# Kernel optimization log

Measured on AMD Instinct MI355X. Metric: run time of the kernel, lower is better.

## Reference

```python
import jax, jax.numpy as jnp
import numpy as np

SEQ, D_IN, H, D_OUT = 8192, 256, 2048, 64


def setup_inputs() -> dict:
    key = jax.random.key(0)
    ks = jax.random.split(key, 9)
    s = 1.0 / np.sqrt(H)  # torch LSTM/Linear init scale
    u = lambda k, shape: jax.random.uniform(k, shape, jnp.float32, -s, s)
    return {
        "x": jax.random.normal(ks[0], (SEQ, D_IN), jnp.float32),
        "hprev": jax.random.normal(ks[1], (1, 1, H), jnp.float32),
        "cprev": jax.random.normal(ks[2], (1, 1, H), jnp.float32),
        "W_ih": u(ks[3], (4 * H, D_IN)),   # gate order: i, f, g, o
        "W_hh": u(ks[4], (4 * H, H)),
        "b_ih": u(ks[5], (4 * H,)),
        "b_hh": u(ks[6], (4 * H,)),
        "W_fc": u(ks[7], (D_OUT, H)),
        "b_fc": u(ks[8], (D_OUT,)),
    }


def _lstm_forward(x, h0, c0, W_ih, W_hh, b_ih, b_hh, W_fc, b_fc):
    # precompute input contributions for all timesteps: [T, 4H]
    xg = x @ W_ih.T + (b_ih + b_hh)
    W_hh_T = W_hh.T  # [H, 4H]

    def step(carry, xg_t):
        h, c = carry
        z = xg_t + h @ W_hh_T  # [4H]
        i, f, g, o = jnp.split(z, 4)
        i = jax.nn.sigmoid(i)
        f = jax.nn.sigmoid(f)
        g = jnp.tanh(g)
        o = jax.nn.sigmoid(o)
        c = f * c + i * g
        h = o * jnp.tanh(c)
        return (h, c), h

    (hT, cT), hs = jax.lax.scan(step, (h0, c0), xg)
    out = jax.nn.sigmoid(hs @ W_fc.T + b_fc)  # [T, D_OUT]
    return out, hT, cT


def reference(x, hprev, cprev, W_ih, W_hh, b_ih, b_hh, W_fc, b_fc):
    out, hT, cT = _lstm_forward(
        x, hprev[0, 0], cprev[0, 0], W_ih, W_hh, b_ih, b_hh, W_fc, b_fc
    )
    return out, hT[None, None, :], cT[None, None, :]
```

## Files before the change

### kernel.cpp

```cpp
#include <hip/hip_runtime.h>
#include <stdint.h>

typedef __fp16 f16x2 __attribute__((ext_vector_type(2)));
typedef __fp16 f16x8 __attribute__((ext_vector_type(8)));
typedef uint32_t u32x4 __attribute__((ext_vector_type(4)));
typedef unsigned long long ull;

#define SEQ  8192
#define HDIM 2048
#define DIN  256
#define DOUT 64

__device__ __forceinline__ f16x2 pk(float lo, float hi) {
    return __builtin_amdgcn_cvt_pkrtz(lo, hi);
}
__device__ __forceinline__ f16x2 pk2(float2 v) { return pk(v.x, v.y); }
__device__ __forceinline__ uint32_t h2u(f16x2 h) { return __builtin_bit_cast(uint32_t, h); }
__device__ __forceinline__ float sigf(float x) { return 1.0f / (1.0f + __expf(-x)); }
__device__ __forceinline__ float tanh_fast(float x) { return 2.0f * sigf(2.0f * x) - 1.0f; }

__device__ __forceinline__ int skH(int j) { return j + 4 * (j >> 7); }
__device__ __forceinline__ int skX(int j) { return j + 4 * (j >> 4); }

__device__ __forceinline__ void ld32_sc1(const ull* p, u32x4& a, u32x4& b) {
    asm volatile("global_load_dwordx4 %0, %2, off sc1\n\t"
                 "global_load_dwordx4 %1, %2, off offset:16 sc1\n\t"
                 "s_waitcnt vmcnt(0)"
                 : "=&v"(a), "=&v"(b) : "v"(p) : "memory");
}
__device__ __forceinline__ u32x4 ld_ctr4(const uint32_t* p) {
    u32x4 v;
    asm volatile("global_load_dwordx4 %0, %1, off sc1\n\t"
                 "s_waitcnt vmcnt(0)"
                 : "=&v"(v) : "v"(p) : "memory");
    return v;
}

__global__ void __launch_bounds__(256, 1)
lstm_persist(const float2* __restrict__ x2,
             const float2* __restrict__ hprev2,
             const float*  __restrict__ cprev,
             const float*  __restrict__ wih,
             const float*  __restrict__ whh,
             const float*  __restrict__ bih,
             const float*  __restrict__ bhh,
             const float2* __restrict__ wfc2,
             const float*  __restrict__ bfc,
             float* __restrict__ out,
             uint32_t* __restrict__ hs_w,
             ull* __restrict__ htag,
             uint32_t* __restrict__ ctr)
{
    const int tid = threadIdx.x;
    const int b   = blockIdx.x;
    const int wv  = tid >> 6;
    const int l   = tid & 63;
    const int g   = l >> 4;
    const int p   = (l >> 3) & 1;
    const int c   = l & 7;

    __shared__ __align__(16) uint32_t smem[12672];
    uint32_t* ldsH0 = smem;
    uint32_t* ldsH1 = smem + 1056;
    uint32_t* ldsX0 = smem + 2112;
    uint32_t* ldsX1 = smem + 2272;
    uint32_t* hsl = smem;
    uint32_t* wfl = smem + 4224;

    uint32_t* hs_priv = hs_w + (size_t)b * 32 * 1024;

    const int unit = 8 * b + 2 * wv + p;
    const int r    = g * 2048 + unit;
    f16x2 wh[128];
    {
        const float4* ptr = (const float4*)(whh + (size_t)r * 2048 + 256 * c);
#pragma unroll
        for (int q = 0; q < 64; ++q) {
            float4 v = ptr[q];
            wh[2*q+0] = pk(v.x, v.y);
            wh[2*q+1] = pk(v.z, v.w);
        }
    }
    f16x2 wx[16];
    {
        const float4* ptr = (const float4*)(wih + (size_t)r * 256 + 32 * c);
#pragma unroll
        for (int q = 0; q < 8; ++q) {
            float4 v = ptr[q];
            wx[2*q+0] = pk(v.x, v.y);
            wx[2*q+1] = pk(v.z, v.w);
        }
    }
#pragma unroll
    for (int k = 0; k < 4; ++k) {
        int j = tid + 256 * k;
        ldsH0[skH(j)] = h2u(pk2(hprev2[j]));
    }
    if (tid < 128) ldsX0[skX(tid)] = h2u(pk2(x2[tid]));
    float2 xw = {0.f, 0.f};
    if (tid < 128) xw = x2[128 + tid];

    float cloc = cprev[unit];
    float hloc = 0.f;
    const float bsum = bih[r] + bhh[r];
    u32x4 prev_pays = {0, 0, 0, 0};
    int  prev_row = 0;
    bool prev_own = false;
    const ull deadline = __builtin_amdgcn_s_memrealtime() + 60000000ull;
    __syncthreads();

    for (int t = 0; t < SEQ; ++t) {
        uint32_t* ldsH  = (t & 1) ? ldsH1 : ldsH0;
        uint32_t* ldsXc = (t & 1) ? ldsX1 : ldsX0;
        uint32_t* ldsXn = (t & 1) ? ldsX0 : ldsX1;

        float accs[8];
#pragma unroll
        for (int q = 0; q < 8; ++q) accs[q] = 0.f;
        {
            const f16x8* xp = (const f16x8*)(ldsXc + 20 * c);
#pragma unroll
            for (int q = 0; q < 4; ++q) {
                f16x8 xv = xp[q];
#pragma unroll
                for (int d = 0; d < 4; ++d) {
                    f16x2 hv = {xv[2*d], xv[2*d+1]};
                    int idx = 4 * q + d;
                    accs[idx & 7] = __builtin_amdgcn_fdot2(wx[idx], hv, accs[idx & 7], false);
                }
            }
        }
        if (tid < 128 && t + 1 < SEQ) ldsXn[skX(tid)] = h2u(pk2(xw));

        if (t > 0) {
            const int par = t & 1;
            const uint32_t target = (uint32_t)((t + (t & 1)) >> 1) * 8u;
            const uint32_t* cbase = ctr + (size_t)par * 8 * 128;
            int spins = 0;
            for (;;) {
                bool ok = true;
                if (l < 8) {
                    u32x4 v = ld_ctr4(cbase + (size_t)l * 128);
                    ok = (v[0] >= target) && (v[1] >= target) &&
                         (v[2] >= target) && (v[3] >= target);
                }
                if (__all(ok)) break;
                if (spins++ > 0) {
                    if (__builtin_amdgcn_s_memrealtime() > deadline) break;
                    __builtin_amdgcn_s_sleep(1);
                }
            }
            const ull* mb = htag + (size_t)par * 1024 + 4 * tid;
            u32x4 qa, qb;
            for (;;) {
                ld32_sc1(mb, qa, qb);
                if (qa[1] == (uint32_t)t && qa[3] == (uint32_t)t &&
                    qb[1] == (uint32_t)t && qb[3] == (uint32_t)t) break;
                if (__builtin_amdgcn_s_memrealtime() > deadline) break;
                __builtin_amdgcn_s_sleep(1);
            }
            u32x4 pays = {qa[0], qa[2], qb[0], qb[2]};
            *(u32x4*)(ldsH + skH(4 * tid)) = pays;
            if (prev_own)
                *(u32x4*)(hs_priv + (size_t)(prev_row & 31) * 1024 + 4 * tid) = prev_pays;
            prev_pays = pays;
            prev_row  = t - 1;
            prev_own  = ((t - 1) >> 5) == b;
        }
        if (tid < 128 && t + 2 < SEQ) xw = x2[(size_t)(t + 2) * 128 + tid];

        __syncthreads();

        {
            const f16x8* hp = (const f16x8*)(ldsH + 132 * c);
#pragma unroll
            for (int q = 0; q < 32; ++q) {
                f16x8 hv8 = hp[q];
#pragma unroll
                for (int d = 0; d < 4; ++d) {
                    f16x2 hh = {hv8[2*d], hv8[2*d+1]};
                    int idx = 4 * q + d;
                    accs[idx & 7] = __builtin_amdgcn_fdot2(wh[idx], hh, accs[idx & 7], false);
                }
            }
        }
        float acc = ((accs[0] + accs[1]) + (accs[2] + accs[3]))
                  + ((accs[4] + accs[5]) + (accs[6] + accs[7]));
        acc += __shfl_xor(acc, 1);
        acc += __shfl_xor(acc, 2);
        acc += __shfl_xor(acc, 4);

        float z = acc + bsum;
        const bool isg = (g == 2);
        float s  = sigf(isg ? 2.0f * z : z);
        float val = isg ? (2.0f * s - 1.0f) : s;
        const int p8 = l & 8;
        float iv = __shfl(val, p8 + 0);
        float fv = __shfl(val, p8 + 16);
        float gv = __shfl(val, p8 + 32);
        float ov = __shfl(val, p8 + 48);
        cloc = fv * cloc + iv * gv;
        hloc = ov * tanh_fast(cloc);

        float h0 = __shfl(hloc, 0);
        float h1 = __shfl(hloc, 8);
        uint32_t pay = h2u(pk(h0, h1));
        if (l == 0) {
            ull tv = ((ull)(uint32_t)(t + 1) << 32) | (ull)pay;
            __hip_atomic_store(htag + (size_t)((t + 1) & 1) * 1024 + 4 * b + wv,
                               tv, __ATOMIC_RELAXED, __HIP_MEMORY_SCOPE_AGENT);
            if (wv == 0)
                atomicAdd(ctr + ((size_t)((t + 1) & 1) * 8 + (b & 7)) * 128 + ((b >> 3) & 3), 1u);
        }
    }

    if (prev_own)
        *(u32x4*)(hs_priv + (size_t)(prev_row & 31) * 1024 + 4 * tid) = prev_pays;

    if (l == 0 || l == 8) {
        out[(size_t)SEQ * DOUT + unit]        = hloc;
        out[(size_t)SEQ * DOUT + HDIM + unit] = cloc;
    }

    if (b == 255) {
        uint32_t pay[4] = {0, 0, 0, 0};
        unsigned got = 0;
        while (got != 0xFu) {
#pragma unroll
            for (int k = 0; k < 4; ++k) {
                if (!(got & (1u << k))) {
                    ull v = __hip_atomic_load(htag + (tid + 256 * k),
                                              __ATOMIC_RELAXED, __HIP_MEMORY_SCOPE_AGENT);
                    if ((uint32_t)(v >> 32) == 8192u) {
                        pay[k] = (uint32_t)v;
                        got |= (1u << k);
                    }
                }
            }
            if (got != 0xFu) {
                if (__builtin_amdgcn_s_memrealtime() > deadline) got = 0xFu;
                __builtin_amdgcn_s_sleep(1);
            }
        }
#pragma unroll
        for (int k = 0; k < 4; ++k)
            hs_priv[(size_t)31 * 1024 + tid + 256 * k] = pay[k];
    }
    __syncthreads();

    const int cc = tid & 63;
    const int rg = tid >> 6;
    const float bo = bfc[cc];
    float fca[8];
#pragma unroll
    for (int q = 0; q < 8; ++q) fca[q] = 0.f;

    for (int ch = 0; ch < 8; ++ch) {
#pragma unroll
        for (int i = 0; i < 16; ++i) {
            int idx = tid + 256 * i;
            int rr = idx >> 7, kp = idx & 127;
            hsl[rr * 132 + kp] = hs_priv[(size_t)rr * 1024 + ch * 128 + kp];
        }
#pragma unroll
        for (int i = 0; i < 32; ++i) {
            int idx = tid + 256 * i;
            int c2 = idx >> 7, kp = idx & 127;
            wfl[c2 * 132 + kp] = h2u(pk2(wfc2[(size_t)c2 * 1024 + ch * 128 + kp]));
        }
        __syncthreads();
#pragma unroll 4
        for (int k4 = 0; k4 < 32; ++k4) {
            f16x8 wvv = *(const f16x8*)(wfl + cc * 132 + 4 * k4);
#pragma unroll
            for (int q = 0; q < 8; ++q) {
                f16x8 hv = *(const f16x8*)(hsl + (rg * 8 + q) * 132 + 4 * k4);
#pragma unroll
                for (int d = 0; d < 4; ++d) {
                    f16x2 a  = {hv[2*d], hv[2*d+1]};
                    f16x2 bb = {wvv[2*d], wvv[2*d+1]};
                    fca[q] = __builtin_amdgcn_fdot2(a, bb, fca[q], false);
                }
            }
        }
        __syncthreads();
    }
#pragma unroll
    for (int q = 0; q < 8; ++q) {
        size_t row = (size_t)32 * b + rg * 8 + q;
        out[row * DOUT + cc] = sigf(fca[q] + bo);
    }
}

extern "C" void kernel_launch(void* const* d_in, const int* in_sizes, int n_in,
                              void* d_out, int out_size, void* d_ws, size_t ws_size,
                              hipStream_t stream) {
    const float2* x2     = (const float2*)d_in[0];
    const float2* hprev2 = (const float2*)d_in[1];
    const float*  cprev  = (const float*)d_in[2];
    const float*  wih    = (const float*)d_in[3];
    const float*  whh    = (const float*)d_in[4];
    const float*  bih    = (const float*)d_in[5];
    const float*  bhh    = (const float*)d_in[6];
    const float2* wfc2   = (const float2*)d_in[7];
    const float*  bfc    = (const float*)d_in[8];
    float*        out    = (float*)d_out;

    char* ws = (char*)d_ws;
    uint32_t* hs_w = (uint32_t*)ws;
    ull*      htag = (ull*)(ws + 33554432);
    uint32_t* ctr  = (uint32_t*)(ws + 33554432 + 16384);

    hipMemsetAsync(ctr, 0, 8192, stream);
    lstm_persist<<<dim3(256), dim3(256), 0, stream>>>(
        x2, hprev2, cprev, wih, whh, bih, bhh, wfc2, bfc,
        out, hs_w, htag, ctr);
}
```

Baseline: 22.54 ms.

## Add dedicated poller wave to spin on global counters and signal workers via LDS

Adds a fifth wavefront to each block whose only job is to poll the global per-step arrival counters. When a step is ready it publishes the step index into an LDS flag. The four compute waves now spin on that cheap LDS flag instead of issuing global counter loads themselves, which is meant to take global polling traffic and latency off the critical path. In exchange, the block grows to 320 threads, which may tighten the per-thread register budget for the large weight arrays held in registers. The poller also joins every per-step barrier, so it cannot poll more than one step ahead.

After: 49.05 ms. 2.18x slower.

```diff
diff --git a/kernel.cpp b/kernel.cpp
--- a/kernel.cpp
+++ b/kernel.cpp
@@ -36,7 +36,7 @@
     return v;
 }
 
-__global__ void __launch_bounds__(256, 1)
+__global__ void __launch_bounds__(320, 1)
 lstm_persist(const float2* __restrict__ x2,
              const float2* __restrict__ hprev2,
              const float*  __restrict__ cprev,
@@ -52,6 +52,7 @@
              uint32_t* __restrict__ ctr)
 {
     const int tid = threadIdx.x;
+    const bool worker = (tid < 256);
     const int b   = blockIdx.x;
     const int wv  = tid >> 6;
     const int l   = tid & 63;
@@ -64,15 +65,20 @@
     uint32_t* ldsH1 = smem + 1056;
     uint32_t* ldsX0 = smem + 2112;
     uint32_t* ldsX1 = smem + 2272;
+    uint32_t* ldsFlag = smem + 2432;
     uint32_t* hsl = smem;
     uint32_t* wfl = smem + 4224;
 
     uint32_t* hs_priv = hs_w + (size_t)b * 32 * 1024;
+
+    if (tid == 0) *ldsFlag = 0;
 
     const int unit = 8 * b + 2 * wv + p;
     const int r    = g * 2048 + unit;
     f16x2 wh[128];
-    {
+    f16x2 wx[16];
+    float cloc = 0.f, bsum = 0.f;
+    if (worker) {
         const float4* ptr = (const float4*)(whh + (size_t)r * 2048 + 256 * c);
 #pragma unroll
         for (int q = 0; q < 64; ++q) {
@@ -80,149 +86,173 @@
             wh[2*q+0] = pk(v.x, v.y);
             wh[2*q+1] = pk(v.z, v.w);
         }
-    }
-    f16x2 wx[16];
-    {
-        const float4* ptr = (const float4*)(wih + (size_t)r * 256 + 32 * c);
+        const float4* ptr2 = (const float4*)(wih + (size_t)r * 256 + 32 * c);
 #pragma unroll
         for (int q = 0; q < 8; ++q) {
-            float4 v = ptr[q];
+            float4 v = ptr2[q];
             wx[2*q+0] = pk(v.x, v.y);
             wx[2*q+1] = pk(v.z, v.w);
         }
-    }
-#pragma unroll
-    for (int k = 0; k < 4; ++k) {
-        int j = tid + 256 * k;
-        ldsH0[skH(j)] = h2u(pk2(hprev2[j]));
+#pragma unroll
+        for (int k = 0; k < 4; ++k) {
+            int j = tid + 256 * k;
+            ldsH0[skH(j)] = h2u(pk2(hprev2[j]));
+        }
+        cloc = cprev[unit];
+        bsum = bih[r] + bhh[r];
     }
     if (tid < 128) ldsX0[skX(tid)] = h2u(pk2(x2[tid]));
     float2 xw = {0.f, 0.f};
     if (tid < 128) xw = x2[128 + tid];
 
-    float cloc = cprev[unit];
     float hloc = 0.f;
-    const float bsum = bih[r] + bhh[r];
     u32x4 prev_pays = {0, 0, 0, 0};
     int  prev_row = 0;
     bool prev_own = false;
     const ull deadline = __builtin_amdgcn_s_memrealtime() + 60000000ull;
     __syncthreads();
 
-    for (int t = 0; t < SEQ; ++t) {
-        uint32_t* ldsH  = (t & 1) ? ldsH1 : ldsH0;
-        uint32_t* ldsXc = (t & 1) ? ldsX1 : ldsX0;
-        uint32_t* ldsXn = (t & 1) ? ldsX0 : ldsX1;
-
-        float accs[8];
-#pragma unroll
-        for (int q = 0; q < 8; ++q) accs[q] = 0.f;
-        {
-            const f16x8* xp = (const f16x8*)(ldsXc + 20 * c);
-#pragma unroll
-            for (int q = 0; q < 4; ++q) {
-                f16x8 xv = xp[q];
-#pragma unroll
-                for (int d = 0; d < 4; ++d) {
-                    f16x2 hv = {xv[2*d], xv[2*d+1]};
-                    int idx = 4 * q + d;
-                    accs[idx & 7] = __builtin_amdgcn_fdot2(wx[idx], hv, accs[idx & 7], false);
-                }
-            }
-        }
-        if (tid < 128 && t + 1 < SEQ) ldsXn[skX(tid)] = h2u(pk2(xw));
-
-        if (t > 0) {
-            const int par = t & 1;
-            const uint32_t target = (uint32_t)((t + (t & 1)) >> 1) * 8u;
-            const uint32_t* cbase = ctr + (size_t)par * 8 * 128;
-            int spins = 0;
-            for (;;) {
-                bool ok = true;
-                if (l < 8) {
-                    u32x4 v = ld_ctr4(cbase + (size_t)l * 128);
-                    ok = (v[0] >= target) && (v[1] >= target) &&
-                         (v[2] >= target) && (v[3] >= target);
-                }
-                if (__all(ok)) break;
-                if (spins++ > 0) {
+    if (!worker) {
+        bool bail = false;
+        __syncthreads();
+        for (int t = 1; t < SEQ; ++t) {
+            if (!bail) {
+                const int par = t & 1;
+                const uint32_t target = (uint32_t)((t + (t & 1)) >> 1) * 8u;
+                const uint32_t* cbase = ctr + (size_t)par * 8 * 128;
+                int spins = 0;
+                for (;;) {
+                    bool ok = true;
+                    if (l < 8) {
+                        u32x4 v = ld_ctr4(cbase + (size_t)l * 128);
+                        ok = (v[0] >= target) && (v[1] >= target) &&
+                             (v[2] >= target) && (v[3] >= target);
+                    }
+                    if (__all(ok)) break;
+                    if (spins++ > 0) {
+                        if (__builtin_amdgcn_s_memrealtime() > deadline) { bail = true; break; }
+                        __builtin_amdgcn_s_sleep(1);
+                    }
+                }
+            }
+            if (l == 0)
+                __hip_atomic_store(ldsFlag, bail ? 0xFFFFFFFFu : (uint32_t)t,
+                                   __ATOMIC_RELAXED, __HIP_MEMORY_SCOPE_WORKGROUP);
+            __syncthreads();
+        }
+    } else {
+        for (int t = 0; t < SEQ; ++t) {
+            uint32_t* ldsH  = (t & 1) ? ldsH1 : ldsH0;
+            uint32_t* ldsXc = (t & 1) ? ldsX1 : ldsX0;
+            uint32_t* ldsXn = (t & 1) ? ldsX0 : ldsX1;
+
+            float accs[8];
+#pragma unroll
+            for (int q = 0; q < 8; ++q) accs[q] = 0.f;
+            {
+                const f16x8* xp = (const f16x8*)(ldsXc + 20 * c);
+#pragma unroll
+                for (int q = 0; q < 4; ++q) {
+                    f16x8 xv = xp[q];
+#pragma unroll
+                    for (int d = 0; d < 4; ++d) {
+                        f16x2 hv = {xv[2*d], xv[2*d+1]};
+                        int idx = 4 * q + d;
+                        accs[idx & 7] = __builtin_amdgcn_fdot2(wx[idx], hv, accs[idx & 7], false);
+                    }
+                }
+            }
+            if (tid < 128 && t + 1 < SEQ) ldsXn[skX(tid)] = h2u(pk2(xw));
+
+            if (t > 0) {
+                const int par = t & 1;
+                {
+                    int spins = 0;
+                    for (;;) {
+                        uint32_t fv = __hip_atomic_load(ldsFlag, __ATOMIC_RELAXED,
+                                                        __HIP_MEMORY_SCOPE_WORKGROUP);
+                        if (fv >= (uint32_t)t) break;
+                        if (++spins > 64) {
+                            spins = 0;
+                            if (__builtin_amdgcn_s_memrealtime() > deadline) break;
+                            __builtin_amdgcn_s_sleep(1);
+                        }
+                    }
+                }
+                const ull* mb = htag + (size_t)par * 1024 + 4 * tid;
+                u32x4 qa, qb;
+                for (;;) {
+                    ld32_sc1(mb, qa, qb);
+                    if (qa[1] == (uint32_t)t && qa[3] == (uint32_t)t &&
+                        qb[1] == (uint32_t)t && qb[3] == (uint32_t)t) break;
                     if (__builtin_amdgcn_s_memrealtime() > deadline) break;
                     __builtin_amdgcn_s_sleep(1);
                 }
-            }
-            const ull* mb = htag + (size_t)par * 1024 + 4 * tid;
-            u32x4 qa, qb;
-            for (;;) {
-                ld32_sc1(mb, qa, qb);
-                if (qa[1] == (uint32_t)t && qa[3] == (uint32_t)t &&
-                    qb[1] == (uint32_t)t && qb[3] == (uint32_t)t) break;
-                if (__builtin_amdgcn_s_memrealtime() > deadline) break;
-                __builtin_amdgcn_s_sleep(1);
-            }
-            u32x4 pays = {qa[0], qa[2], qb[0], qb[2]};
-            *(u32x4*)(ldsH + skH(4 * tid)) = pays;
-            if (prev_own)
-                *(u32x4*)(hs_priv + (size_t)(prev_row & 31) * 1024 + 4 * tid) = prev_pays;
-            prev_pays = pays;
-            prev_row  = t - 1;
-            prev_own  = ((t - 1) >> 5) == b;
-        }
-        if (tid < 128 && t + 2 < SEQ) xw = x2[(size_t)(t + 2) * 128 + tid];
-
-        __syncthreads();
-
-        {
-            const f16x8* hp = (const f16x8*)(ldsH + 132 * c);
-#pragma unroll
-            for (int q = 0; q < 32; ++q) {
-                f16x8 hv8 = hp[q];
-#pragma unroll
-                for (int d = 0; d < 4; ++d) {
-                    f16x2 hh = {hv8[2*d], hv8[2*d+1]};
-                    int idx = 4 * q + d;
-                    accs[idx & 7] = __builtin_amdgcn_fdot2(wh[idx], hh, accs[idx & 7], false);
-                }
-            }
-        }
-        float acc = ((accs[0] + accs[1]) + (accs[2] + accs[3]))
-                  + ((accs[4] + accs[5]) + (accs[6] + accs[7]));
-        acc += __shfl_xor(acc, 1);
-        acc += __shfl_xor(acc, 2);
-        acc += __shfl_xor(acc, 4);
-
-        float z = acc + bsum;
-        const bool isg = (g == 2);
-        float s  = sigf(isg ? 2.0f * z : z);
-        float val = isg ? (2.0f * s - 1.0f) : s;
-        const int p8 = l & 8;
-        float iv = __shfl(val, p8 + 0);
-        float fv = __shfl(val, p8 + 16);
-        float gv = __shfl(val, p8 + 32);
-        float ov = __shfl(val, p8 + 48);
-        cloc = fv * cloc + iv * gv;
-        hloc = ov * tanh_fast(cloc);
-
-        float h0 = __shfl(hloc, 0);
-        float h1 = __shfl(hloc, 8);
-        uint32_t pay = h2u(pk(h0, h1));
-        if (l == 0) {
-            ull tv = ((ull)(uint32_t)(t + 1) << 32) | (ull)pay;
-            __hip_atomic_store(htag + (size_t)((t + 1) & 1) * 1024 + 4 * b + wv,
-                               tv, __ATOMIC_RELAXED, __HIP_MEMORY_SCOPE_AGENT);
-            if (wv == 0)
-                atomicAdd(ctr + ((size_t)((t + 1) & 1) * 8 + (b & 7)) * 128 + ((b >> 3) & 3), 1u);
+                u32x4 pays = {qa[0], qa[2], qb[0], qb[2]};
+                *(u32x4*)(ldsH + skH(4 * tid)) = pays;
+                if (prev_own)
+                    *(u32x4*)(hs_priv + (size_t)(prev_row & 31) * 1024 + 4 * tid) = prev_pays;
+                prev_pays = pays;
+                prev_row  = t - 1;
+                prev_own  = ((t - 1) >> 5) == b;
+            }
+            if (tid < 128 && t + 2 < SEQ) xw = x2[(size_t)(t + 2) * 128 + tid];
+
+            __syncthreads();
+
+            {
+                const f16x8* hp = (const f16x8*)(ldsH + 132 * c);
+#pragma unroll
+                for (int q = 0; q < 32; ++q) {
+                    f16x8 hv8 = hp[q];
+#pragma unroll
+                    for (int d = 0; d < 4; ++d) {
+                        f16x2 hh = {hv8[2*d], hv8[2*d+1]};
+                        int idx = 4 * q + d;
+                        accs[idx & 7] = __builtin_amdgcn_fdot2(wh[idx], hh, accs[idx & 7], false);
+                    }
+                }
+            }
+            float acc = ((accs[0] + accs[1]) + (accs[2] + accs[3]))
+                      + ((accs[4] + accs[5]) + (accs[6] + accs[7]));
+            acc += __shfl_xor(acc, 1);
+            acc += __shfl_xor(acc, 2);
+            acc += __shfl_xor(acc, 4);
+
+            float z = acc + bsum;
+            const bool isg = (g == 2);
+            float s  = sigf(isg ? 2.0f * z : z);
+            float val = isg ? (2.0f * s - 1.0f) : s;
+            const int p8 = l & 8;
+            float iv = __shfl(val, p8 + 0);
+            float fv = __shfl(val, p8 + 16);
+            float gv = __shfl(val, p8 + 32);
+            float ov = __shfl(val, p8 + 48);
+            cloc = fv * cloc + iv * gv;
+            hloc = ov * tanh_fast(cloc);
+
+            float h0 = __shfl(hloc, 0);
+            float h1 = __shfl(hloc, 8);
+            uint32_t pay = h2u(pk(h0, h1));
+            if (l == 0) {
+                ull tv = ((ull)(uint32_t)(t + 1) << 32) | (ull)pay;
+                __hip_atomic_store(htag + (size_t)((t + 1) & 1) * 1024 + 4 * b + wv,
+                                   tv, __ATOMIC_RELAXED, __HIP_MEMORY_SCOPE_AGENT);
+                if (wv == 0)
+                    atomicAdd(ctr + ((size_t)((t + 1) & 1) * 8 + (b & 7)) * 128 + ((b >> 3) & 3), 1u);
+            }
         }
     }
 
     if (prev_own)
         *(u32x4*)(hs_priv + (size_t)(prev_row & 31) * 1024 + 4 * tid) = prev_pays;
 
-    if (l == 0 || l == 8) {
+    if (worker && (l == 0 || l == 8)) {
         out[(size_t)SEQ * DOUT + unit]        = hloc;
         out[(size_t)SEQ * DOUT + HDIM + unit] = cloc;
     }
 
-    if (b == 255) {
+    if (b == 255 && worker) {
         uint32_t pay[4] = {0, 0, 0, 0};
         unsigned got = 0;
         while (got != 0xFu) {
@@ -256,39 +286,45 @@
     for (int q = 0; q < 8; ++q) fca[q] = 0.f;
 
     for (int ch = 0; ch < 8; ++ch) {
-#pragma unroll
-        for (int i = 0; i < 16; ++i) {
-            int idx = tid + 256 * i;
-            int rr = idx >> 7, kp = idx & 127;
-            hsl[rr * 132 + kp] = hs_priv[(size_t)rr * 1024 + ch * 128 + kp];
-        }
-#pragma unroll
-        for (int i = 0; i < 32; ++i) {
-            int idx = tid + 256 * i;
-            int c2 = idx >> 7, kp = idx & 127;
-            wfl[c2 * 132 + kp] = h2u(pk2(wfc2[(size_t)c2 * 1024 + ch * 128 + kp]));
+        if (worker) {
+#pragma unroll
+            for (int i = 0; i < 16; ++i) {
+                int idx = tid + 256 * i;
+                int rr = idx >> 7, kp = idx & 127;
+                hsl[rr * 132 + kp] = hs_priv[(size_t)rr * 1024 + ch * 128 + kp];
+            }
+#pragma unroll
+            for (int i = 0; i < 32; ++i) {
+                int idx = tid + 256 * i;
+                int c2 = idx >> 7, kp = idx & 127;
+                wfl[c2 * 132 + kp] = h2u(pk2(wfc2[(size_t)c2 * 1024 + ch * 128 + kp]));
+            }
         }
         __syncthreads();
+        if (worker) {
 #pragma unroll 4
-        for (int k4 = 0; k4 < 32; ++k4) {
-            f16x8 wvv = *(const f16x8*)(wfl + cc * 132 + 4 * k4);
-#pragma unroll
-            for (int q = 0; q < 8; ++q) {
-                f16x8 hv = *(const f16x8*)(hsl + (rg * 8 + q) * 132 + 4 * k4);
-#pragma unroll
-                for (int d = 0; d < 4; ++d) {
-                    f16x2 a  = {hv[2*d], hv[2*d+1]};
-                    f16x2 bb = {wvv[2*d], wvv[2*d+1]};
-                    fca[q] = __builtin_amdgcn_fdot2(a, bb, fca[q], false);
+            for (int k4 = 0; k4 < 32; ++k4) {
+                f16x8 wvv = *(const f16x8*)(wfl + cc * 132 + 4 * k4);
+#pragma unroll
+                for (int q = 0; q < 8; ++q) {
+                    f16x8 hv = *(const f16x8*)(hsl + (rg * 8 + q) * 132 + 4 * k4);
+#pragma unroll
+                    for (int d = 0; d < 4; ++d) {
+                        f16x2 a  = {hv[2*d], hv[2*d+1]};
+                        f16x2 bb = {wvv[2*d], wvv[2*d+1]};
+                        fca[q] = __builtin_amdgcn_fdot2(a, bb, fca[q], false);
+                    }
                 }
             }
         }
         __syncthreads();
     }
-#pragma unroll
-    for (int q = 0; q < 8; ++q) {
-        size_t row = (size_t)32 * b + rg * 8 + q;
-        out[row * DOUT + cc] = sigf(fca[q] + bo);
+    if (worker) {
+#pragma unroll
+        for (int q = 0; q < 8; ++q) {
+            size_t row = (size_t)32 * b + rg * 8 + q;
+            out[row * DOUT + cc] = sigf(fca[q] + bo);
+        }
     }
 }
 
@@ -312,7 +348,7 @@
     uint32_t* ctr  = (uint32_t*)(ws + 33554432 + 16384);
 
     hipMemsetAsync(ctr, 0, 8192, stream);
-    lstm_persist<<<dim3(256), dim3(256), 0, stream>>>(
+    lstm_persist<<<dim3(256), dim3(320), 0, stream>>>(
         x2, hprev2, cprev, wih, whh, bih, bhh, wfc2, bfc,
         out, hs_w, htag, ctr);
 }
```
